# Kernel optimization log

Hardware: AMD Instinct MI355X
Metric: run time of the kernel (lower is better)

Reference implementation:

```python
import jax, jax.numpy as jnp
import numpy as np
from math import sqrt

T, B, V = 32, 16, 30000
D, DQKV = 300, 150
K, G = 10, 32            # top-K globals, grapharea_size neighbours each
S = 25000                # last_idx_senses (= SC rows)
EPS = 1e-8


def setup_inputs() -> dict:
    key = jax.random.key(0)
    ks = jax.random.split(key, 6)
    return {
        "predictions_globals": jax.random.normal(ks[0], (T, B, V), jnp.float32),
        "location_context": jax.random.normal(ks[1], (T, B, D), jnp.float32),
        "SC": jax.random.normal(ks[2], (S, D), jnp.float32),
        "Wq": jax.random.normal(ks[3], (D, DQKV), jnp.float32) / sqrt(D),
        "Wk": jax.random.normal(ks[4], (D, DQKV), jnp.float32) / sqrt(D),
        "neighbours_table": jax.random.randint(ks[5], (V, G), 0, S, jnp.int64),
    }


def reference(predictions_globals, location_context, SC, Wq, Wk, neighbours_table):
    # 1) per-sample top-K global selection (sort descending, take K indices)
    _, topk_idx = jax.lax.top_k(predictions_globals, K)          # [T,B,K]
    # 2) sense-neighbour lookup: K globals x G neighbours -> N = K*G senses
    neigh = neighbours_table[topk_idx].reshape(T, B, K * G)      # [T,B,N] int
    # 3) gather precomputed sense contexts
    senses_context = SC[neigh]                                   # [T,B,N,D]
    # 4) ComputeLogits: QK attention logits
    q = location_context @ Wq                                    # [T,B,dqkv]
    k = senses_context @ Wk                                      # [T,B,N,dqkv]
    logits = jnp.einsum("tbd,tbnd->tbn", q, k) / sqrt(DQKV)      # [T,B,N]
    # 5) softmax over neighbours, scatter into full sense distribution
    p = jax.nn.softmax(logits, axis=-1)                          # [T,B,N]
    base = jnp.full((T * B, S), EPS, dtype=p.dtype)
    rows = jnp.arange(T * B)[:, None]                            # [TB,1]
    senses_softmax = base.at[rows, neigh.reshape(T * B, -1)].set(p.reshape(T * B, -1))
    # 6) log-probabilities over all senses
    return jnp.log(senses_softmax)                               # [T*B, S]
```

## Files before the change

kernel.cpp:

```cpp
#include <hip/hip_runtime.h>
#include <math.h>

#define T_ 32
#define B_ 16
#define V_ 30000
#define V4 7500
#define D_ 300
#define DQKV_ 150
#define K_ 10
#define G_ 32
#define N_ 320
#define S_ 25000
#define S4 6250
#define SLICE 3125
#define QKP 304
#define NTS 1024
#define NTG 256
#define NTF 384
#define LCAP 4096
#define UTH 0xC0000000u

__device__ __forceinline__ unsigned umap(float f) {
    unsigned b = __float_as_uint(f);
    unsigned mask = (unsigned)(((int)b) >> 31);
    return b ^ (mask | 0x80000000u);
}
__device__ __forceinline__ bool better_u(unsigned au, int ai, unsigned bu, int bi) {
    return (au > bu) || (au == bu && ai < bi);
}

__global__ __launch_bounds__(NTS, 2) void scan_prep_kernel(
    const float* __restrict__ pred, const float* __restrict__ lc,
    const float* __restrict__ Wq, const float* __restrict__ Wk,
    const int* __restrict__ nbt,
    float* __restrict__ out, float* __restrict__ qkws, int* __restrict__ nidxws)
{
    const int row = blockIdx.x, tid = threadIdx.x;
    const int lane = tid & 63, wave = tid >> 6;
    __shared__ unsigned lu[LCAP];
    __shared__ int      li[LCAP];
    __shared__ int      cnt;
    __shared__ int      topg[K_];
    __shared__ __align__(16) float lcs[D_];
    __shared__ float    qpart[4][DQKV_];

    if (tid == 0) cnt = 0;
    __syncthreads();

    const float FILL = -18.420680743952367f;
    {
        float4 f4 = make_float4(FILL, FILL, FILL, FILL);
        float4* o4 = (float4*)(out + (size_t)row * S_);
        #pragma unroll
        for (int k = 0; k < 7; ++k) { int i = tid + k * NTS; if (i < S4) o4[i] = f4; }
    }

    {
        const float4* p4 = (const float4*)(pred + (size_t)row * V_);
        #pragma unroll
        for (int k = 0; k < 8; ++k) {
            int i = tid + k * NTS;
            if (i < V4) {
                float4 v = p4[i];
                unsigned u0 = umap(v.x), u1 = umap(v.y), u2 = umap(v.z), u3 = umap(v.w);
                int base = i * 4;
                if (u0 >= UTH) { int p = atomicAdd(&cnt, 1); if (p < LCAP) { lu[p] = u0; li[p] = base; } }
                if (u1 >= UTH) { int p = atomicAdd(&cnt, 1); if (p < LCAP) { lu[p] = u1; li[p] = base + 1; } }
                if (u2 >= UTH) { int p = atomicAdd(&cnt, 1); if (p < LCAP) { lu[p] = u2; li[p] = base + 2; } }
                if (u3 >= UTH) { int p = atomicAdd(&cnt, 1); if (p < LCAP) { lu[p] = u3; li[p] = base + 3; } }
            }
        }
    }
    __syncthreads();
    const int c = cnt;

    if (c >= K_ && c <= LCAP) {
        if (wave == 0) {
            for (int p = 0; p < K_; ++p) {
                unsigned bu = 0; int bi = 0x7fffffff;
                for (int s = lane; s < c; s += 64) {
                    unsigned uu = lu[s]; int ii = li[s];
                    if (better_u(uu, ii, bu, bi)) { bu = uu; bi = ii; }
                }
                #pragma unroll
                for (int off = 32; off; off >>= 1) {
                    unsigned ou = __shfl_xor(bu, off, 64);
                    int      oi = __shfl_xor(bi, off, 64);
                    if (better_u(ou, oi, bu, bi)) { bu = ou; bi = oi; }
                }
                if (lane == 0) topg[p] = bi;
                for (int s = lane; s < c; s += 64)
                    if (li[s] == bi && lu[s] == bu) lu[s] = 0;
            }
        }
    } else {
        if (wave == 0) {
            unsigned tu[K_]; int tix[K_];
            #pragma unroll
            for (int s = 0; s < K_; ++s) { tu[s] = 0; tix[s] = 0x7fffffff; }
            const float* prow = pred + (size_t)row * V_;
            for (int i = lane; i < V_; i += 64) {
                unsigned u = umap(prow[i]);
                if (better_u(u, i, tu[K_-1], tix[K_-1])) {
                    tu[K_-1] = u; tix[K_-1] = i;
                    #pragma unroll
                    for (int s = K_-1; s > 0; --s)
                        if (better_u(tu[s], tix[s], tu[s-1], tix[s-1])) {
                            unsigned a = tu[s]; tu[s] = tu[s-1]; tu[s-1] = a;
                            int b2 = tix[s]; tix[s] = tix[s-1]; tix[s-1] = b2;
                        }
                }
            }
            for (int p = 0; p < K_; ++p) {
                unsigned bu = tu[0]; int bi = tix[0];
                #pragma unroll
                for (int s = 1; s < K_; ++s)
                    if (better_u(tu[s], tix[s], bu, bi)) { bu = tu[s]; bi = tix[s]; }
                #pragma unroll
                for (int off = 32; off; off >>= 1) {
                    unsigned ou = __shfl_xor(bu, off, 64);
                    int      oi = __shfl_xor(bi, off, 64);
                    if (better_u(ou, oi, bu, bi)) { bu = ou; bi = oi; }
                }
                if (lane == 0) topg[p] = bi;
                #pragma unroll
                for (int s = 0; s < K_; ++s)
                    if (tix[s] == bi) tu[s] = 0;
            }
        }
    }
    __syncthreads();

    if (tid < N_) nidxws[(size_t)row * N_ + tid] = nbt[topg[tid >> 5] * G_ + (tid & 31)];
    if (tid >= 384 && tid < 384 + D_ / 4)
        ((float4*)lcs)[tid - 384] = ((const float4*)(lc + (size_t)row * D_))[tid - 384];
    __syncthreads();

    if (tid < 4 * DQKV_) {
        int h = tid / DQKV_;
        int j = tid - h * DQKV_;
        int d0 = h * 75;
        const float* wp = Wq + (size_t)d0 * DQKV_ + j;
        float acc = 0.f;
        #pragma unroll 5
        for (int dd = 0; dd < 75; ++dd)
            acc += lcs[d0 + dd] * wp[(size_t)dd * DQKV_];
        qpart[h][j] = acc;
    }
    __syncthreads();

    {
        float qv0 = qpart[0][lane] + qpart[1][lane] + qpart[2][lane] + qpart[3][lane];
        float qv1 = qpart[0][64 + lane] + qpart[1][64 + lane] + qpart[2][64 + lane] + qpart[3][64 + lane];
        float qv2 = (lane < 22) ? (qpart[0][128 + lane] + qpart[1][128 + lane]
                                 + qpart[2][128 + lane] + qpart[3][128 + lane]) : 0.f;
        for (int d = wave; d < D_; d += 16) {
            const float* wr = Wk + (size_t)d * DQKV_;
            float w0 = wr[lane];
            float w1 = wr[64 + lane];
            float w2 = (lane < 22) ? wr[128 + lane] : 0.f;
            float p = w0 * qv0 + w1 * qv1 + w2 * qv2;
            #pragma unroll
            for (int off = 32; off; off >>= 1) p += __shfl_xor(p, off, 64);
            if (lane == 0) qkws[(size_t)row * QKP + d] = p;
        }
    }
}

__global__ __launch_bounds__(NTG) void gather_kernel(
    const float* __restrict__ SC, const float* __restrict__ qkws,
    const int* __restrict__ nidxws, float* __restrict__ logws)
{
    const int r = blockIdx.x >> 3;
    const int ch = blockIdx.x & 7;
    const int lo = ch * SLICE, hi = lo + SLICE;
    const int tid = threadIdx.x;
    __shared__ int   nid[N_];
    __shared__ __align__(16) float qk[D_];
    __shared__ int   list[N_];
    __shared__ int   lcnt;

    if (tid == 0) lcnt = 0;
    for (int i = tid; i < N_; i += NTG)
        nid[i] = nidxws[(size_t)r * N_ + i];
    if (tid < D_ / 4)
        ((float4*)qk)[tid] = ((const float4*)(qkws + (size_t)r * QKP))[tid];
    __syncthreads();

    for (int i = tid; i < N_; i += NTG) {
        int sv = nid[i];
        if (sv >= lo && sv < hi) { int p = atomicAdd(&lcnt, 1); list[p] = i; }
    }
    __syncthreads();
    const int c2 = lcnt;

    const float ISC = 0.08164965809277260327f;
    const float4* q4 = (const float4*)qk;
    for (int s = tid; s < 8 * c2; s += NTG) {
        int g = s >> 3, h = s & 7;
        int n = list[g];
        const float4* sc4 = (const float4*)(SC + (size_t)nid[n] * D_);
        int c0 = h * 9;
        float acc = 0.f;
        #pragma unroll
        for (int cc = 0; cc < 9; ++cc) {
            float4 a = sc4[c0 + cc];
            float4 b = q4[c0 + cc];
            acc += a.x * b.x + a.y * b.y + a.z * b.z + a.w * b.w;
        }
        if (h < 3) {
            float4 a = sc4[72 + h];
            float4 b = q4[72 + h];
            acc += a.x * b.x + a.y * b.y + a.z * b.z + a.w * b.w;
        }
        acc += __shfl_xor(acc, 1, 64);
        acc += __shfl_xor(acc, 2, 64);
        acc += __shfl_xor(acc, 4, 64);
        if (h == 0) logws[(size_t)r * N_ + n] = acc * ISC;
    }
}

__global__ __launch_bounds__(NTF) void finalize_kernel(
    const float* __restrict__ logws, const int* __restrict__ nidxws,
    float* __restrict__ out)
{
    const int row = blockIdx.x, tid = threadIdx.x;
    const int lane = tid & 63, wave = tid >> 6;
    __shared__ float lg[N_];
    __shared__ int   nid[N_];
    __shared__ int   kills[N_];
    __shared__ float redA[6], redB[6];
    float* outrow = out + (size_t)row * S_;

    if (tid < N_) {
        lg[tid]  = logws[(size_t)row * N_ + tid];
        nid[tid] = nidxws[(size_t)row * N_ + tid];
        kills[tid] = 0;
    }
    __syncthreads();

    float v = (tid < N_) ? lg[tid] : -INFINITY;
    float m = v;
    #pragma unroll
    for (int off = 32; off; off >>= 1) m = fmaxf(m, __shfl_xor(m, off, 64));
    if (lane == 0) redA[wave] = m;
    __syncthreads();
    m = redA[0];
    #pragma unroll
    for (int w = 1; w < 6; ++w) m = fmaxf(m, redA[w]);

    float ss = (tid < N_) ? expf(v - m) : 0.f;
    #pragma unroll
    for (int off = 32; off; off >>= 1) ss += __shfl_xor(ss, off, 64);
    if (lane == 0) redB[wave] = ss;
    __syncthreads();
    float tot = redB[0];
    #pragma unroll
    for (int w = 1; w < 6; ++w) tot += redB[w];
    float lsum = logf(tot);

    for (int s = tid; s < 4 * N_; s += NTF) {
        int n = s >> 2, cix = s & 3;
        int sidx = nid[n];
        int clo = cix * 80;
        int lo2 = (n + 1 > clo) ? n + 1 : clo;
        int hi2 = clo + 80;
        bool mt = false;
        #pragma unroll 4
        for (int n2 = lo2; n2 < hi2; ++n2) mt |= (nid[n2] == sidx);
        if (mt) kills[n] = 1;
    }
    __syncthreads();

    if (tid < N_ && !kills[tid]) outrow[nid[tid]] = (v - m) - lsum;
}

#define NWS 16
__device__ __forceinline__ bool better(float av, int ai, float bv, int bi) {
    return (av > bv) || (av == bv && ai < bi);
}
__global__ __launch_bounds__(NTS, 4) void selfatt_fused(
    const float* __restrict__ pred, const float* __restrict__ lc,
    const float* __restrict__ SC, const float* __restrict__ Wq,
    const float* __restrict__ Wk, const int* __restrict__ nbt,
    float* __restrict__ out)
{
    const int row = blockIdx.x, tid = threadIdx.x;
    const int lane = tid & 63, wave = tid >> 6;
    __shared__ float wcv[NWS * K_];
    __shared__ int   wci[NWS * K_];
    __shared__ int   topg[K_];
    __shared__ float lcs[D_];
    __shared__ float qs[DQKV_];
    __shared__ __align__(16) float qks[D_];
    __shared__ int   nidx[N_];
    __shared__ float lg[N_];
    __shared__ int   kills[N_];
    __shared__ float redA[NWS], redB[NWS];
    float* outrow = out + (size_t)row * S_;
    const float FILL = -18.420680743952367f;
    {
        float4 f4 = make_float4(FILL, FILL, FILL, FILL);
        float4* o4 = (float4*)outrow;
        #pragma unroll
        for (int k = 0; k < 7; ++k) { int i = tid + k * NTS; if (i < S4) o4[i] = f4; }
    }
    float tv[K_]; int ti[K_];
    #pragma unroll
    for (int s = 0; s < K_; ++s) { tv[s] = -INFINITY; ti[s] = 0x7fffffff; }
    {
        const float4* p4 = (const float4*)(pred + (size_t)row * V_);
        const float4 NEG = make_float4(-INFINITY, -INFINITY, -INFINITY, -INFINITY);
        float4 a[8]; int ib[8];
        #pragma unroll
        for (int u = 0; u < 8; ++u) {
            int i = tid + u * NTS;
            a[u]  = (i < V4) ? p4[i] : NEG;
            ib[u] = (i < V4) ? i * 4 : 0x7ffffff0;
        }
        #pragma unroll
        for (int u = 0; u < 8; ++u) {
            float x = a[u].x, y = a[u].y, z = a[u].z, w = a[u].w;
            float m4 = fmaxf(fmaxf(x, y), fmaxf(z, w));
            if (!(m4 < tv[K_-1])) {
                float vals[4] = {x, y, z, w};
                #pragma unroll
                for (int cc = 0; cc < 4; ++cc) {
                    float val = vals[cc];
                    int   idx = ib[u] + cc;
                    if (better(val, idx, tv[K_-1], ti[K_-1])) {
                        tv[K_-1] = val; ti[K_-1] = idx;
                        #pragma unroll
                        for (int s = K_-1; s > 0; --s) {
                            if (better(tv[s], ti[s], tv[s-1], ti[s-1])) {
                                float fx = tv[s]; tv[s] = tv[s-1]; tv[s-1] = fx;
                                int   iy = ti[s]; ti[s] = ti[s-1]; ti[s-1] = iy;
                            }
                        }
                    }
                }
            }
        }
    }
    for (int p = 0; p < K_; ++p) {
        float bv = tv[0]; int bi = ti[0];
        #pragma unroll
        for (int s = 1; s < K_; ++s)
            if (better(tv[s], ti[s], bv, bi)) { bv = tv[s]; bi = ti[s]; }
        #pragma unroll
        for (int off = 32; off; off >>= 1) {
            float ov = __shfl_xor(bv, off, 64);
            int   oi = __shfl_xor(bi, off, 64);
            if (better(ov, oi, bv, bi)) { bv = ov; bi = oi; }
        }
        if (lane == 0) { wcv[wave * K_ + p] = bv; wci[wave * K_ + p] = bi; }
        #pragma unroll
        for (int s = 0; s < K_; ++s)
            if (ti[s] == bi) tv[s] = -INFINITY;
    }
    __syncthreads();
    if (wave == 0) {
        float c0v = wcv[lane],      c1v = wcv[64 + lane];
        int   c0i = wci[lane],      c1i = wci[64 + lane];
        float c2v = (lane < 32) ? wcv[128 + lane] : -INFINITY;
        int   c2i = (lane < 32) ? wci[128 + lane] : 0x7fffffff;
        for (int p = 0; p < K_; ++p) {
            float bv = c0v; int bi = c0i;
            if (better(c1v, c1i, bv, bi)) { bv = c1v; bi = c1i; }
            if (better(c2v, c2i, bv, bi)) { bv = c2v; bi = c2i; }
            #pragma unroll
            for (int off = 32; off; off >>= 1) {
                float ov = __shfl_xor(bv, off, 64);
                int   oi = __shfl_xor(bi, off, 64);
                if (better(ov, oi, bv, bi)) { bv = ov; bi = oi; }
            }
            if (lane == 0) topg[p] = bi;
            if (c0i == bi) c0v = -INFINITY;
            if (c1i == bi) c1v = -INFINITY;
            if (c2i == bi) c2v = -INFINITY;
        }
    }
    __syncthreads();
    if (tid < N_) { int g = topg[tid >> 5]; nidx[tid] = nbt[g * G_ + (tid & 31)]; }
    else if (tid < 2 * N_) kills[tid - N_] = 0;
    else if (tid >= 640 && tid < 640 + D_) lcs[tid - 640] = lc[(size_t)row * D_ + (tid - 640)];
    __syncthreads();
    if (tid < 600) {
        int j = tid >> 2, h = tid & 3;
        int d0 = h * 75;
        const float* wp = Wq + (size_t)d0 * DQKV_ + j;
        float acc = 0.f;
        #pragma unroll 5
        for (int dd = 0; dd < 75; ++dd) acc += lcs[d0 + dd] * wp[(size_t)dd * DQKV_];
        acc += __shfl_xor(acc, 1, 64);
        acc += __shfl_xor(acc, 2, 64);
        if (h == 0) qs[j] = acc;
    } else {
        int t0 = tid - 600;
        for (int s = t0; s < 4 * N_; s += 424) {
            int n = s >> 2, cc = s & 3;
            int sidx = nidx[n];
            int clo = cc * 80;
            int lo = (n + 1 > clo) ? n + 1 : clo;
            int hi = clo + 80;
            bool mt = false;
            #pragma unroll 4
            for (int n2 = lo; n2 < hi; ++n2) mt |= (nidx[n2] == sidx);
            if (mt) kills[n] = 1;
        }
    }
    __syncthreads();
    if (tid < 600) {
        int d = tid >> 1, h = tid & 1;
        int j0 = h * 75;
        const float* wrow = Wk + (size_t)d * DQKV_ + j0;
        float acc = 0.f;
        #pragma unroll 5
        for (int jj = 0; jj < 75; ++jj) acc += wrow[jj] * qs[j0 + jj];
        acc += __shfl_xor(acc, 1, 64);
        if (h == 0) qks[d] = acc;
    }
    __syncthreads();
    const float ISC = 0.08164965809277260327f;
    const float4* q4 = (const float4*)qks;
    for (int s = tid; s < 8 * N_; s += NTS) {
        int n = s >> 3, h = s & 7;
        const float4* sc4 = (const float4*)(SC + (size_t)nidx[n] * D_);
        int c0 = h * 9;
        float acc = 0.f;
        #pragma unroll
        for (int cc = 0; cc < 9; ++cc) {
            float4 a = sc4[c0 + cc];
            float4 b = q4[c0 + cc];
            acc += a.x * b.x + a.y * b.y + a.z * b.z + a.w * b.w;
        }
        if (h < 3) {
            float4 a = sc4[72 + h];
            float4 b = q4[72 + h];
            acc += a.x * b.x + a.y * b.y + a.z * b.z + a.w * b.w;
        }
        acc += __shfl_xor(acc, 1, 64);
        acc += __shfl_xor(acc, 2, 64);
        acc += __shfl_xor(acc, 4, 64);
        if (h == 0) lg[n] = acc * ISC;
    }
    __syncthreads();
    float v = (tid < N_) ? lg[tid] : -INFINITY;
    float m = v;
    #pragma unroll
    for (int off = 32; off; off >>= 1) m = fmaxf(m, __shfl_xor(m, off, 64));
    if (lane == 0) redA[wave] = m;
    __syncthreads();
    m = redA[0];
    #pragma unroll
    for (int w = 1; w < NWS; ++w) m = fmaxf(m, redA[w]);
    float e = (tid < N_) ? expf(v - m) : 0.f;
    float ss = e;
    #pragma unroll
    for (int off = 32; off; off >>= 1) ss += __shfl_xor(ss, off, 64);
    if (lane == 0) redB[wave] = ss;
    __syncthreads();
    float tot = redB[0];
    #pragma unroll
    for (int w = 1; w < NWS; ++w) tot += redB[w];
    float lsum = logf(tot);
    if (tid < N_ && !kills[tid]) outrow[nidx[tid]] = (v - m) - lsum;
}

extern "C" void kernel_launch(void* const* d_in, const int* in_sizes, int n_in,
                              void* d_out, int out_size, void* d_ws, size_t ws_size,
                              hipStream_t stream) {
    const float* pred = (const float*)d_in[0];
    const float* lc   = (const float*)d_in[1];
    const float* SC   = (const float*)d_in[2];
    const float* Wq   = (const float*)d_in[3];
    const float* Wk   = (const float*)d_in[4];
    const int*   nbt  = (const int*)d_in[5];
    float* out = (float*)d_out;

    const int nrows = T_ * B_;
    const size_t nQK = (size_t)nrows * QKP;
    const size_t nNI = (size_t)nrows * N_;
    const size_t nLG = (size_t)nrows * N_;
    const size_t need = (nQK + nLG) * sizeof(float) + nNI * sizeof(int);

    if (ws_size >= need) {
        float* qkws   = (float*)d_ws;
        int*   nidxws = (int*)(qkws + nQK);
        float* logws  = (float*)(nidxws + nNI);
        scan_prep_kernel<<<dim3(nrows), dim3(NTS), 0, stream>>>(
            pred, lc, Wq, Wk, nbt, out, qkws, nidxws);
        gather_kernel<<<dim3(nrows * 8), dim3(NTG), 0, stream>>>(
            SC, qkws, nidxws, logws);
        finalize_kernel<<<dim3(nrows), dim3(NTF), 0, stream>>>(
            logws, nidxws, out);
    } else {
        selfatt_fused<<<dim3(T_ * B_), dim3(NTS), 0, stream>>>(
            pred, lc, SC, Wq, Wk, nbt, out);
    }
}
```

Baseline: 126.5 us.

## Split scan_prep kernel into separate top-k scan and q/qk prep kernels

The fused scan+prep kernel is split in two. The first does the fill and top-k and writes the K indices to a workspace buffer. A new 512-thread prep kernel reads them back, then builds the neighbour index lists and computes q and Wk·q with the Wq dot split two ways instead of four. The aim is to stop the big scan kernel from carrying prep's shared memory and registers, and to run prep with fewer threads, at the cost of an extra launch and a global round-trip for the top-k indices.

```diff
diff --git a/kernel.cpp b/kernel.cpp
--- a/kernel.cpp
+++ b/kernel.cpp
@@ -15,6 +15,7 @@
 #define SLICE 3125
 #define QKP 304
 #define NTS 1024
+#define NTP 512
 #define NTG 256
 #define NTF 384
 #define LCAP 4096
@@ -29,20 +30,15 @@
     return (au > bu) || (au == bu && ai < bi);
 }
 
-__global__ __launch_bounds__(NTS, 2) void scan_prep_kernel(
-    const float* __restrict__ pred, const float* __restrict__ lc,
-    const float* __restrict__ Wq, const float* __restrict__ Wk,
-    const int* __restrict__ nbt,
-    float* __restrict__ out, float* __restrict__ qkws, int* __restrict__ nidxws)
+__global__ __launch_bounds__(NTS, 2) void scan_kernel(
+    const float* __restrict__ pred, float* __restrict__ out,
+    int* __restrict__ wstop)
 {
     const int row = blockIdx.x, tid = threadIdx.x;
     const int lane = tid & 63, wave = tid >> 6;
     __shared__ unsigned lu[LCAP];
     __shared__ int      li[LCAP];
     __shared__ int      cnt;
-    __shared__ int      topg[K_];
-    __shared__ __align__(16) float lcs[D_];
-    __shared__ float    qpart[4][DQKV_];
 
     if (tid == 0) cnt = 0;
     __syncthreads();
@@ -88,7 +84,7 @@
                     int      oi = __shfl_xor(bi, off, 64);
                     if (better_u(ou, oi, bu, bi)) { bu = ou; bi = oi; }
                 }
-                if (lane == 0) topg[p] = bi;
+                if (lane == 0) wstop[row * K_ + p] = bi;
                 for (int s = lane; s < c; s += 64)
                     if (li[s] == bi && lu[s] == bu) lu[s] = 0;
             }
@@ -122,39 +118,54 @@
                     int      oi = __shfl_xor(bi, off, 64);
                     if (better_u(ou, oi, bu, bi)) { bu = ou; bi = oi; }
                 }
-                if (lane == 0) topg[p] = bi;
+                if (lane == 0) wstop[row * K_ + p] = bi;
                 #pragma unroll
                 for (int s = 0; s < K_; ++s)
                     if (tix[s] == bi) tu[s] = 0;
             }
         }
     }
+}
+
+__global__ __launch_bounds__(NTP, 2) void prep_kernel(
+    const float* __restrict__ lc, const float* __restrict__ Wq,
+    const float* __restrict__ Wk, const int* __restrict__ nbt,
+    const int* __restrict__ wstop,
+    float* __restrict__ qkws, int* __restrict__ nidxws)
+{
+    const int row = blockIdx.x, tid = threadIdx.x;
+    const int lane = tid & 63, wave = tid >> 6;
+    __shared__ int   topg[K_];
+    __shared__ __align__(16) float lcs[D_];
+    __shared__ float qpart[2][DQKV_];
+
+    if (tid < K_) topg[tid] = wstop[row * K_ + tid];
+    if (tid >= 64 && tid < 64 + D_ / 4)
+        ((float4*)lcs)[tid - 64] = ((const float4*)(lc + (size_t)row * D_))[tid - 64];
     __syncthreads();
 
     if (tid < N_) nidxws[(size_t)row * N_ + tid] = nbt[topg[tid >> 5] * G_ + (tid & 31)];
-    if (tid >= 384 && tid < 384 + D_ / 4)
-        ((float4*)lcs)[tid - 384] = ((const float4*)(lc + (size_t)row * D_))[tid - 384];
-    __syncthreads();
-
-    if (tid < 4 * DQKV_) {
+
+    if (tid < 2 * DQKV_) {
         int h = tid / DQKV_;
         int j = tid - h * DQKV_;
-        int d0 = h * 75;
+        int d0 = h * 150;
         const float* wp = Wq + (size_t)d0 * DQKV_ + j;
-        float acc = 0.f;
+        float a0 = 0.f, a1 = 0.f;
         #pragma unroll 5
-        for (int dd = 0; dd < 75; ++dd)
-            acc += lcs[d0 + dd] * wp[(size_t)dd * DQKV_];
-        qpart[h][j] = acc;
+        for (int dd = 0; dd < 150; dd += 2) {
+            a0 += lcs[d0 + dd]     * wp[(size_t)dd * DQKV_];
+            a1 += lcs[d0 + dd + 1] * wp[(size_t)(dd + 1) * DQKV_];
+        }
+        qpart[h][j] = a0 + a1;
     }
     __syncthreads();
 
     {
-        float qv0 = qpart[0][lane] + qpart[1][lane] + qpart[2][lane] + qpart[3][lane];
-        float qv1 = qpart[0][64 + lane] + qpart[1][64 + lane] + qpart[2][64 + lane] + qpart[3][64 + lane];
-        float qv2 = (lane < 22) ? (qpart[0][128 + lane] + qpart[1][128 + lane]
-                                 + qpart[2][128 + lane] + qpart[3][128 + lane]) : 0.f;
-        for (int d = wave; d < D_; d += 16) {
+        float qv0 = qpart[0][lane] + qpart[1][lane];
+        float qv1 = qpart[0][64 + lane] + qpart[1][64 + lane];
+        float qv2 = (lane < 22) ? (qpart[0][128 + lane] + qpart[1][128 + lane]) : 0.f;
+        for (int d = wave; d < D_; d += 8) {
             const float* wr = Wk + (size_t)d * DQKV_;
             float w0 = wr[lane];
             float w1 = wr[64 + lane];
@@ -482,14 +493,17 @@
     const size_t nQK = (size_t)nrows * QKP;
     const size_t nNI = (size_t)nrows * N_;
     const size_t nLG = (size_t)nrows * N_;
-    const size_t need = (nQK + nLG) * sizeof(float) + nNI * sizeof(int);
+    const size_t nTP = (size_t)nrows * K_;
+    const size_t need = (nQK + nLG) * sizeof(float) + (nNI + nTP) * sizeof(int);
 
     if (ws_size >= need) {
         float* qkws   = (float*)d_ws;
         int*   nidxws = (int*)(qkws + nQK);
         float* logws  = (float*)(nidxws + nNI);
-        scan_prep_kernel<<<dim3(nrows), dim3(NTS), 0, stream>>>(
-            pred, lc, Wq, Wk, nbt, out, qkws, nidxws);
+        int*   wstop  = (int*)(logws + nLG);
+        scan_kernel<<<dim3(nrows), dim3(NTS), 0, stream>>>(pred, out, wstop);
+        prep_kernel<<<dim3(nrows), dim3(NTP), 0, stream>>>(
+            lc, Wq, Wk, nbt, wstop, qkws, nidxws);
         gather_kernel<<<dim3(nrows * 8), dim3(NTG), 0, stream>>>(
             SC, qkws, nidxws, logws);
         finalize_kernel<<<dim3(nrows), dim3(NTF), 0, stream>>>(
```

New measurement: 110.1 us. -12.9%, faster.
